# Optimization experiments

Hardware: AMD Instinct MI355X
Metric: run time of the kernel (lower is better)

Reference implementation:

```python
import jax, jax.numpy as jnp
import numpy as np

DIM = 768
HEADS = 12
SCALE = DIM ** (-0.5)  # NOTE: original scales by full dim, not per-head dim


def setup_inputs() -> dict:
    key = jax.random.key(0)
    k1, k2, k3 = jax.random.split(key, 3)
    b, n = 4, 2048
    x = jax.random.normal(k1, (b, n, DIM), dtype=jnp.float32)
    # torch Linear layout: weight [out_features, in_features]
    w_qkv = jax.random.normal(k2, (3 * DIM, DIM), dtype=jnp.float32) * (DIM ** -0.5)
    b_qkv = jnp.zeros((3 * DIM,), dtype=jnp.float32)
    w_out = jax.random.normal(k3, (DIM, DIM), dtype=jnp.float32) * (DIM ** -0.5)
    b_out = jnp.zeros((DIM,), dtype=jnp.float32)
    return {"x": x, "w_qkv": w_qkv, "b_qkv": b_qkv, "w_out": w_out, "b_out": b_out}


def reference(x, w_qkv, b_qkv, w_out, b_out):
    b, n, dim = x.shape
    h = HEADS
    d = dim // h
    qkv = x @ w_qkv.T + b_qkv                       # [b, n, 3*dim]
    # rearrange 'b n (qkv h d) -> qkv b h n d'
    qkv = qkv.reshape(b, n, 3, h, d).transpose(2, 0, 3, 1, 4)
    q, k, v = qkv[0], qkv[1], qkv[2]                # each [b, h, n, d]
    dots = jnp.einsum('bhid,bhjd->bhij', q, k) * SCALE
    attn = jax.nn.softmax(dots, axis=-1)
    out = jnp.einsum('bhij,bhjd->bhid', attn, v)    # [b, h, n, d]
    out = out.transpose(0, 2, 1, 3).reshape(b, n, h * d)
    out = out @ w_out.T + b_out
    return out
```

## Files before the change

kernel.cpp:

```cpp
#include <hip/hip_runtime.h>
#include <hip/hip_bf16.h>
#include <stdint.h>
#include <math.h>

#define HEADS 12
#define HD 64
#define NB 4
#define NSEQ 2048
#define DIM 768
#define MROWS (NB*NSEQ)
#define QKV_OUT (3*DIM)
#define QSCALE (0.03608439182435161f * 1.4426950408889634f)

typedef __bf16 bf16;
typedef __attribute__((ext_vector_type(8))) __bf16 bf16x8;
typedef __attribute__((ext_vector_type(4))) __bf16 bf16x4;
typedef __attribute__((ext_vector_type(4))) float f32x4;
typedef __attribute__((ext_vector_type(16))) float f32x16;
typedef unsigned int uint;

typedef __attribute__((address_space(1))) void gvoid_t;
typedef __attribute__((address_space(3))) void lvoid_t;
#define GLOAD_LDS16(src, dst) \
  __builtin_amdgcn_global_load_lds((gvoid_t*)(src), (lvoid_t*)(dst), 16, 0, 0)

__device__ __forceinline__ float fast_exp2(float x) {
  float r; asm("v_exp_f32 %0, %1" : "=v"(r) : "v"(x)); return r;
}
__device__ __forceinline__ uint cvtpk_bf16(float a, float b) {
  uint r; asm("v_cvt_pk_bf16_f32 %0, %1, %2" : "=v"(r) : "v"(a), "v"(b)); return r;
}
__device__ __forceinline__ void plswap(uint &a, uint &b) {
  asm("v_permlane32_swap_b32 %0, %1" : "+v"(a), "+v"(b));
}

__global__ void k_cvt3(const float* __restrict__ x, const float* __restrict__ wqkv,
                       const float* __restrict__ wout,
                       bf16* __restrict__ xb, bf16* __restrict__ wqkvb,
                       bf16* __restrict__ woutb) {
  const int n0 = MROWS * DIM / 4, n1 = QKV_OUT * DIM / 4, n2 = DIM * DIM / 4;
  int i = blockIdx.x * blockDim.x + threadIdx.x;
  const float* src; bf16* dst;
  if (i < n0)           { src = x;    dst = xb; }
  else if (i < n0 + n1) { src = wqkv; dst = wqkvb; i -= n0; }
  else if (i < n0 + n1 + n2) { src = wout; dst = woutb; i -= n0 + n1; }
  else return;
  const f32x4 v = ((const f32x4*)src)[i];
  bf16x4 o;
#pragma unroll
  for (int j = 0; j < 4; ++j) o[j] = (bf16)v[j];
  ((bf16x4*)dst)[i] = o;
}

template<int ROWBYTES>
__device__ __forceinline__ void stage_swz(const bf16* g, int grow0, int gstride,
                                          int gcol0, char* ldsbuf) {
  constexpr int CPR = ROWBYTES / 16;
  const int t = threadIdx.x;
  const int wid = t >> 6;
#pragma unroll
  for (int call = 0; call < 2; ++call) {
    const int o = call * 4096 + t * 16;
    const int r = o / ROWBYTES;
    const int c = (o % ROWBYTES) / 16;
    const int cs = c ^ (r & (CPR - 1));
    const bf16* src = g + (long)(grow0 + r) * gstride + gcol0 + cs * 8;
    char* dst = ldsbuf + call * 4096 + wid * 1024;
    GLOAD_LDS16(src, dst);
  }
}

template<int ROWBYTES>
__device__ __forceinline__ bf16x8 frag_ld(const char* buf, int row, int chunk) {
  constexpr int CPR = ROWBYTES / 16;
  const int cs = chunk ^ (row & (CPR - 1));
  return *(const bf16x8*)(buf + row * ROWBYTES + cs * 16);
}

__device__ __forceinline__ void build_pfrags(const f32x16 &p, bf16x8 *f) {
  union { uint u[4]; bf16x8 v; } A, B;
  uint a0 = cvtpk_bf16(p[0], p[1]),  b0 = cvtpk_bf16(p[4], p[5]);   plswap(a0, b0);
  uint a1 = cvtpk_bf16(p[2], p[3]),  b1 = cvtpk_bf16(p[6], p[7]);   plswap(a1, b1);
  A.u[0] = a0; A.u[1] = a1; A.u[2] = b0; A.u[3] = b1;
  uint a2 = cvtpk_bf16(p[8], p[9]),  b2 = cvtpk_bf16(p[12], p[13]); plswap(a2, b2);
  uint a3 = cvtpk_bf16(p[10], p[11]), b3 = cvtpk_bf16(p[14], p[15]); plswap(a3, b3);
  B.u[0] = a2; B.u[1] = a3; B.u[2] = b2; B.u[3] = b3;
  f[0] = A.v; f[1] = B.v;
}

__device__ __forceinline__ void gemm_core(const bf16* __restrict__ A, const bf16* __restrict__ Bm,
                                          int m0, int n0, f32x4 acc[4][4], char* lds) {
  const int t = threadIdx.x;
  const int lane = t & 63, wid = t >> 6;
  const int lr = lane & 15, l4 = lane >> 4;
  const int wm = wid >> 1, wn = wid & 1;
#pragma unroll
  for (int i = 0; i < 4; ++i)
#pragma unroll
    for (int j = 0; j < 4; ++j) acc[i][j] = f32x4{0.f, 0.f, 0.f, 0.f};

  stage_swz<64>(A, m0, DIM, 0, lds);
  stage_swz<64>(Bm, n0, DIM, 0, lds + 16384);
  __syncthreads();
  int cur = 0;
  const int NT = DIM / 32;
  for (int kt = 0; kt < NT; ++kt) {
    char* Acur = lds + cur * 8192;
    char* Bcur = lds + 16384 + cur * 8192;
    if (kt + 1 < NT) {
      stage_swz<64>(A, m0, DIM, (kt + 1) * 32, lds + (cur ^ 1) * 8192);
      stage_swz<64>(Bm, n0, DIM, (kt + 1) * 32, lds + 16384 + (cur ^ 1) * 8192);
    }
    bf16x8 af[4], bfr[4];
#pragma unroll
    for (int i = 0; i < 4; ++i) af[i] = frag_ld<64>(Acur, wm * 64 + i * 16 + lr, l4);
#pragma unroll
    for (int j = 0; j < 4; ++j) bfr[j] = frag_ld<64>(Bcur, wn * 64 + j * 16 + lr, l4);
#pragma unroll
    for (int i = 0; i < 4; ++i)
#pragma unroll
      for (int j = 0; j < 4; ++j)
        acc[i][j] = __builtin_amdgcn_mfma_f32_16x16x32_bf16(af[i], bfr[j], acc[i][j], 0, 0, 0);
    __syncthreads();
    cur ^= 1;
  }
}

__global__ void __launch_bounds__(256) k_qkv_gemm(const bf16* __restrict__ xb,
                                                  const bf16* __restrict__ wb,
                                                  const float* __restrict__ bqkv,
                                                  bf16* __restrict__ qb,
                                                  bf16* __restrict__ kb,
                                                  bf16* __restrict__ vtb) {
  __shared__ alignas(128) char lds[32768];
  const int m0 = blockIdx.x * 128;
  const int n0 = blockIdx.y * 128;
  const int region = n0 / DIM;
  const int t = threadIdx.x;
  const int lane = t & 63, wid = t >> 6;
  const int lr = lane & 15, l4 = lane >> 4;
  const int wm = wid >> 1, wn = wid & 1;
  f32x4 acc[4][4];

  if (region < 2) {
    gemm_core(wb, xb, n0, m0, acc, lds);
    bf16* dst0 = (region == 0) ? qb : kb;
#pragma unroll
    for (int j = 0; j < 4; ++j) {
      const int mb = m0 + wn * 64 + j * 16 + lr;
      const int bb = mb >> 11, nn = mb & 2047;
#pragma unroll
      for (int i = 0; i < 4; ++i) {
        const int o = n0 + wm * 64 + i * 16 + l4 * 4;
        const f32x4 b4 = *(const f32x4*)(bqkv + o);
        const int oc = o - region * DIM;
        const int h = oc >> 6, d = oc & 63;
        bf16x4 pk;
#pragma unroll
        for (int r = 0; r < 4; ++r) {
          float v = acc[i][j][r] + b4[r];
          if (region == 0) v *= QSCALE;
          pk[r] = (bf16)v;
        }
        *(bf16x4*)(dst0 + ((long)((bb * HEADS + h) * NSEQ + nn)) * HD + d) = pk;
      }
    }
  } else {
    gemm_core(xb, wb, m0, n0, acc, lds);
#pragma unroll
    for (int j = 0; j < 4; ++j) {
      const int o = n0 + wn * 64 + j * 16 + lr;
      const float bias = bqkv[o];
      const int oc = o - 2 * DIM;
      const int h = oc >> 6, d = oc & 63;
#pragma unroll
      for (int i = 0; i < 4; ++i) {
        const int mb = m0 + wm * 64 + i * 16 + l4 * 4;
        const int bb = mb >> 11, nn = mb & 2047;
        bf16x4 pk;
#pragma unroll
        for (int r = 0; r < 4; ++r) pk[r] = (bf16)(acc[i][j][r] + bias);
        *(bf16x4*)(vtb + ((long)((bb * HEADS + h) * HD + d)) * NSEQ + nn) = pk;
      }
    }
  }
}

__global__ void __launch_bounds__(256) k_attn(const bf16* __restrict__ qb,
                                              const bf16* __restrict__ kb,
                                              const bf16* __restrict__ vtb,
                                              bf16* __restrict__ ob) {
  __shared__ alignas(128) char lds[32768];
  char* ldsc = lds;
  const int bh = blockIdx.x;
  const int qt = blockIdx.y;
  const int t = threadIdx.x;
  const int lane = t & 63, wid = t >> 6;
  const int l31 = lane & 31, hi = lane >> 5;
  const bf16* qg = qb + (long)bh * NSEQ * HD;
  const bf16* kg = kb + (long)bh * NSEQ * HD;
  const bf16* vg = vtb + (long)bh * HD * NSEQ;
  const int q0w = qt * 128 + wid * 32;

  bf16x8 bq[4];
#pragma unroll
  for (int ks = 0; ks < 4; ++ks)
    bq[ks] = *(const bf16x8*)(qg + (long)(q0w + l31) * HD + ks * 16 + hi * 8);

  const int rbase = l31 * 128 + (((hi ^ l31) & 7) << 4);

  const int o0 = t * 16, o1 = 4096 + t * 16;
  const int r0 = o0 >> 7, cs0 = ((o0 & 127) >> 4) ^ (r0 & 7);
  const int r1 = o1 >> 7, cs1 = ((o1 & 127) >> 4) ^ (r1 & 7);
  const bf16* ksA = kg + r0 * 64 + cs0 * 8;
  const bf16* ksB = kg + r1 * 64 + cs1 * 8;
  const bf16* vsA = vg + (long)r0 * NSEQ + cs0 * 8;
  const bf16* vsB = vg + (long)r1 * NSEQ + cs1 * 8;
  const int dofs = wid << 10;

  f32x16 ot0, ot1;
#pragma unroll
  for (int r = 0; r < 16; ++r) { ot0[r] = 0.f; ot1[r] = 0.f; }
  float l_run = 0.f;

  GLOAD_LDS16(ksA, ldsc + dofs);
  GLOAD_LDS16(ksB, ldsc + 4096 + dofs);
  GLOAD_LDS16(vsA, ldsc + 16384 + dofs);
  GLOAD_LDS16(vsB, ldsc + 20480 + dofs);
  __syncthreads();
  int cur = 0;
  for (int kt = 0; kt < NSEQ / 64; ++kt) {
    if (kt + 1 < NSEQ / 64) {
      const int nb = (cur ^ 1) << 13;
      const int ko = (kt + 1) * 4096;
      const int vo = (kt + 1) * 64;
      GLOAD_LDS16(ksA + ko, ldsc + nb + dofs);
      GLOAD_LDS16(ksB + ko, ldsc + nb + 4096 + dofs);
      GLOAD_LDS16(vsA + vo, ldsc + nb + 16384 + dofs);
      GLOAD_LDS16(vsB + vo, ldsc + nb + 20480 + dofs);
    }
    const int tb = rbase + (cur << 13);
    f32x16 s0, s1;
#pragma unroll
    for (int r = 0; r < 16; ++r) { s0[r] = 0.f; s1[r] = 0.f; }
    __builtin_amdgcn_s_setprio(1);
#pragma unroll
    for (int ks = 0; ks < 4; ++ks) {
      const int a = tb ^ (ks << 5);
      const bf16x8 ak0 = *(const bf16x8*)(ldsc + a);
      s0 = __builtin_amdgcn_mfma_f32_32x32x16_bf16(ak0, bq[ks], s0, 0, 0, 0);
      const bf16x8 ak1 = *(const bf16x8*)(ldsc + a + 4096);
      s1 = __builtin_amdgcn_mfma_f32_32x32x16_bf16(ak1, bq[ks], s1, 0, 0, 0);
    }
    __builtin_amdgcn_s_setprio(0);
    float rs0 = 0.f, rs1 = 0.f;
#pragma unroll
    for (int r = 0; r < 16; ++r) {
      s0[r] = fast_exp2(s0[r]); rs0 += s0[r];
      s1[r] = fast_exp2(s1[r]); rs1 += s1[r];
    }
    l_run += rs0 + rs1;
    bf16x8 pf[4];
    build_pfrags(s0, &pf[0]);
    build_pfrags(s1, &pf[2]);
    __builtin_amdgcn_s_setprio(1);
#pragma unroll
    for (int s = 0; s < 4; ++s) {
      const int a = tb ^ (s << 5);
      const bf16x8 av0 = *(const bf16x8*)(ldsc + a + 16384);
      ot0 = __builtin_amdgcn_mfma_f32_32x32x16_bf16(av0, pf[s], ot0, 0, 0, 0);
      const bf16x8 av1 = *(const bf16x8*)(ldsc + a + 20480);
      ot1 = __builtin_amdgcn_mfma_f32_32x32x16_bf16(av1, pf[s], ot1, 0, 0, 0);
    }
    __builtin_amdgcn_s_setprio(0);
    __syncthreads();
    cur ^= 1;
  }
  l_run += __shfl_xor(l_run, 32);
  const float inv = 1.f / l_run;
#pragma unroll
  for (int r = 0; r < 16; ++r) { ot0[r] *= inv; ot1[r] *= inv; }
  __syncthreads();
  char* tw = lds + wid * 4352;
#pragma unroll
  for (int g = 0; g < 4; ++g) {
    uint2 w0, w1;
    w0.x = cvtpk_bf16(ot0[4 * g], ot0[4 * g + 1]);
    w0.y = cvtpk_bf16(ot0[4 * g + 2], ot0[4 * g + 3]);
    w1.x = cvtpk_bf16(ot1[4 * g], ot1[4 * g + 1]);
    w1.y = cvtpk_bf16(ot1[4 * g + 2], ot1[4 * g + 3]);
    const int d0 = 8 * g + 4 * hi;
    *(uint2*)(tw + l31 * 136 + d0 * 2) = w0;
    *(uint2*)(tw + l31 * 136 + (32 + d0) * 2) = w1;
  }
  const int b_ = bh / HEADS, h_ = bh - b_ * HEADS;
#pragma unroll
  for (int pass = 0; pass < 4; ++pass) {
    const int row = pass * 8 + (lane >> 3);
    const bf16x8 vv = *(const bf16x8*)(tw + row * 136 + (lane & 7) * 16);
    *(bf16x8*)(ob + ((long)(b_ * NSEQ + q0w + row)) * DIM + h_ * 64 + (lane & 7) * 8) = vv;
  }
}

__global__ void __launch_bounds__(256) k_out_gemm(const bf16* __restrict__ ab,
                                                  const bf16* __restrict__ wob,
                                                  const float* __restrict__ bout,
                                                  float* __restrict__ out) {
  __shared__ alignas(128) char lds[32768];
  const int m0 = blockIdx.x * 128;
  const int n0 = blockIdx.y * 128;
  f32x4 acc[4][4];
  gemm_core(wob, ab, n0, m0, acc, lds);

  const int t = threadIdx.x;
  const int lane = t & 63, wid = t >> 6;
  const int lr = lane & 15, l4 = lane >> 4;
  const int wm = wid >> 1, wn = wid & 1;
#pragma unroll
  for (int j = 0; j < 4; ++j) {
    const int mb = m0 + wn * 64 + j * 16 + lr;
#pragma unroll
    for (int i = 0; i < 4; ++i) {
      const int o = n0 + wm * 64 + i * 16 + l4 * 4;
      const f32x4 v = acc[i][j] + *(const f32x4*)(bout + o);
      *(f32x4*)(out + (long)mb * DIM + o) = v;
    }
  }
}

extern "C" void kernel_launch(void* const* d_in, const int* in_sizes, int n_in,
                              void* d_out, int out_size, void* d_ws, size_t ws_size,
                              hipStream_t stream) {
  const float* x    = (const float*)d_in[0];
  const float* wqkv = (const float*)d_in[1];
  const float* bqkv = (const float*)d_in[2];
  const float* wout = (const float*)d_in[3];
  const float* bout = (const float*)d_in[4];
  float* out = (float*)d_out;
  char* ws = (char*)d_ws;

  bf16* xb    = (bf16*)(ws);
  bf16* wqkvb = (bf16*)(ws + 12582912);
  bf16* woutb = (bf16*)(ws + 16121856);
  bf16* qb    = (bf16*)(ws + 17301504);
  bf16* kb    = (bf16*)(ws + 29884416);
  bf16* vtb   = (bf16*)(ws + 42467328);
  bf16* ab    = (bf16*)(ws + 55050240);

  const int ncvt4 = MROWS * DIM / 4 + QKV_OUT * DIM / 4 + DIM * DIM / 4;
  k_cvt3<<<(ncvt4 + 255) / 256, 256, 0, stream>>>(x, wqkv, wout, xb, wqkvb, woutb);

  k_qkv_gemm<<<dim3(MROWS / 128, QKV_OUT / 128), 256, 0, stream>>>(xb, wqkvb, bqkv, qb, kb, vtb);
  k_attn<<<dim3(NB * HEADS, NSEQ / 128), 256, 0, stream>>>(qb, kb, vtb, ab);
  k_out_gemm<<<dim3(MROWS / 128, DIM / 128), 256, 0, stream>>>(ab, woutb, bout, out);
}
```

Baseline: 153.0 us.

## Software-pipeline attention loop with triple-buffered K/V and overlapped QK^T

Restructures the attention kernel's main loop so the QK^T MFMAs for the next key tile are issued alongside the exp/PV work for the current tile. K and V now each get three LDS slots, with loads staged two or three tiles ahead under explicit vmcnt waits and raw barriers instead of full __syncthreads. The aim is to hide global-load latency and the softmax VALU work behind matrix work. In exchange, LDS per block grows from 32 KB to 48 KB and an extra pair of score accumulators raises register use, both of which can lower occupancy.

```diff
diff --git a/kernel.cpp b/kernel.cpp
--- a/kernel.cpp
+++ b/kernel.cpp
@@ -88,6 +88,47 @@
   f[0] = A.v; f[1] = B.v;
 }
 
+__device__ __forceinline__ void qkt_step(const char* ldsc, int rbase, int kslot,
+                                         const bf16x8 bq[4], f32x16 &P0, f32x16 &P1) {
+#pragma unroll
+  for (int r = 0; r < 16; ++r) { P0[r] = 0.f; P1[r] = 0.f; }
+  __builtin_amdgcn_s_setprio(1);
+#pragma unroll
+  for (int ks = 0; ks < 4; ++ks) {
+    const int a = (rbase ^ (ks << 5)) + kslot * 8192;
+    const bf16x8 ak0 = *(const bf16x8*)(ldsc + a);
+    P0 = __builtin_amdgcn_mfma_f32_32x32x16_bf16(ak0, bq[ks], P0, 0, 0, 0);
+    const bf16x8 ak1 = *(const bf16x8*)(ldsc + a + 4096);
+    P1 = __builtin_amdgcn_mfma_f32_32x32x16_bf16(ak1, bq[ks], P1, 0, 0, 0);
+  }
+  __builtin_amdgcn_s_setprio(0);
+}
+
+__device__ __forceinline__ void smpv_step(const char* ldsc, int rbase, int vslot,
+                                          f32x16 &C0, f32x16 &C1, f32x16 &ot0, f32x16 &ot1,
+                                          float &l_run) {
+  float rs0 = 0.f, rs1 = 0.f;
+#pragma unroll
+  for (int r = 0; r < 16; ++r) {
+    C0[r] = fast_exp2(C0[r]); rs0 += C0[r];
+    C1[r] = fast_exp2(C1[r]); rs1 += C1[r];
+  }
+  l_run += rs0 + rs1;
+  bf16x8 pf[4];
+  build_pfrags(C0, &pf[0]);
+  build_pfrags(C1, &pf[2]);
+  __builtin_amdgcn_s_setprio(1);
+#pragma unroll
+  for (int s = 0; s < 4; ++s) {
+    const int a = (rbase ^ (s << 5)) + 24576 + vslot * 8192;
+    const bf16x8 av0 = *(const bf16x8*)(ldsc + a);
+    ot0 = __builtin_amdgcn_mfma_f32_32x32x16_bf16(av0, pf[s], ot0, 0, 0, 0);
+    const bf16x8 av1 = *(const bf16x8*)(ldsc + a + 4096);
+    ot1 = __builtin_amdgcn_mfma_f32_32x32x16_bf16(av1, pf[s], ot1, 0, 0, 0);
+  }
+  __builtin_amdgcn_s_setprio(0);
+}
+
 __device__ __forceinline__ void gemm_core(const bf16* __restrict__ A, const bf16* __restrict__ Bm,
                                           int m0, int n0, f32x4 acc[4][4], char* lds) {
   const int t = threadIdx.x;
@@ -190,7 +231,7 @@
                                               const bf16* __restrict__ kb,
                                               const bf16* __restrict__ vtb,
                                               bf16* __restrict__ ob) {
-  __shared__ alignas(128) char lds[32768];
+  __shared__ alignas(128) char lds[49152];
   char* ldsc = lds;
   const int bh = blockIdx.x;
   const int qt = blockIdx.y;
@@ -210,77 +251,62 @@
   const int rbase = l31 * 128 + (((hi ^ l31) & 7) << 4);
 
   const int o0 = t * 16, o1 = 4096 + t * 16;
-  const int r0 = o0 >> 7, cs0 = ((o0 & 127) >> 4) ^ (r0 & 7);
-  const int r1 = o1 >> 7, cs1 = ((o1 & 127) >> 4) ^ (r1 & 7);
-  const bf16* ksA = kg + r0 * 64 + cs0 * 8;
-  const bf16* ksB = kg + r1 * 64 + cs1 * 8;
-  const bf16* vsA = vg + (long)r0 * NSEQ + cs0 * 8;
-  const bf16* vsB = vg + (long)r1 * NSEQ + cs1 * 8;
+  const int r0i = o0 >> 7, cs0 = ((o0 & 127) >> 4) ^ (r0i & 7);
+  const int r1i = o1 >> 7, cs1 = ((o1 & 127) >> 4) ^ (r1i & 7);
+  const bf16* ksA = kg + r0i * 64 + cs0 * 8;
+  const bf16* ksB = kg + r1i * 64 + cs1 * 8;
+  const bf16* vsA = vg + (long)r0i * NSEQ + cs0 * 8;
+  const bf16* vsB = vg + (long)r1i * NSEQ + cs1 * 8;
   const int dofs = wid << 10;
+
+  auto stage_k = [&](int j, int slot) {
+    GLOAD_LDS16(ksA + j * 4096, ldsc + slot * 8192 + dofs);
+    GLOAD_LDS16(ksB + j * 4096, ldsc + slot * 8192 + 4096 + dofs);
+  };
+  auto stage_v = [&](int j, int slot) {
+    GLOAD_LDS16(vsA + j * 64, ldsc + 24576 + slot * 8192 + dofs);
+    GLOAD_LDS16(vsB + j * 64, ldsc + 24576 + slot * 8192 + 4096 + dofs);
+  };
 
   f32x16 ot0, ot1;
 #pragma unroll
   for (int r = 0; r < 16; ++r) { ot0[r] = 0.f; ot1[r] = 0.f; }
   float l_run = 0.f;
 
-  GLOAD_LDS16(ksA, ldsc + dofs);
-  GLOAD_LDS16(ksB, ldsc + 4096 + dofs);
-  GLOAD_LDS16(vsA, ldsc + 16384 + dofs);
-  GLOAD_LDS16(vsB, ldsc + 20480 + dofs);
-  __syncthreads();
-  int cur = 0;
-  for (int kt = 0; kt < NSEQ / 64; ++kt) {
-    if (kt + 1 < NSEQ / 64) {
-      const int nb = (cur ^ 1) << 13;
-      const int ko = (kt + 1) * 4096;
-      const int vo = (kt + 1) * 64;
-      GLOAD_LDS16(ksA + ko, ldsc + nb + dofs);
-      GLOAD_LDS16(ksB + ko, ldsc + nb + 4096 + dofs);
-      GLOAD_LDS16(vsA + vo, ldsc + nb + 16384 + dofs);
-      GLOAD_LDS16(vsB + vo, ldsc + nb + 20480 + dofs);
-    }
-    const int tb = rbase + (cur << 13);
-    f32x16 s0, s1;
-#pragma unroll
-    for (int r = 0; r < 16; ++r) { s0[r] = 0.f; s1[r] = 0.f; }
-    __builtin_amdgcn_s_setprio(1);
-#pragma unroll
-    for (int ks = 0; ks < 4; ++ks) {
-      const int a = tb ^ (ks << 5);
-      const bf16x8 ak0 = *(const bf16x8*)(ldsc + a);
-      s0 = __builtin_amdgcn_mfma_f32_32x32x16_bf16(ak0, bq[ks], s0, 0, 0, 0);
-      const bf16x8 ak1 = *(const bf16x8*)(ldsc + a + 4096);
-      s1 = __builtin_amdgcn_mfma_f32_32x32x16_bf16(ak1, bq[ks], s1, 0, 0, 0);
-    }
-    __builtin_amdgcn_s_setprio(0);
-    float rs0 = 0.f, rs1 = 0.f;
-#pragma unroll
-    for (int r = 0; r < 16; ++r) {
-      s0[r] = fast_exp2(s0[r]); rs0 += s0[r];
-      s1[r] = fast_exp2(s1[r]); rs1 += s1[r];
-    }
-    l_run += rs0 + rs1;
-    bf16x8 pf[4];
-    build_pfrags(s0, &pf[0]);
-    build_pfrags(s1, &pf[2]);
-    __builtin_amdgcn_s_setprio(1);
-#pragma unroll
-    for (int s = 0; s < 4; ++s) {
-      const int a = tb ^ (s << 5);
-      const bf16x8 av0 = *(const bf16x8*)(ldsc + a + 16384);
-      ot0 = __builtin_amdgcn_mfma_f32_32x32x16_bf16(av0, pf[s], ot0, 0, 0, 0);
-      const bf16x8 av1 = *(const bf16x8*)(ldsc + a + 20480);
-      ot1 = __builtin_amdgcn_mfma_f32_32x32x16_bf16(av1, pf[s], ot1, 0, 0, 0);
-    }
-    __builtin_amdgcn_s_setprio(0);
-    __syncthreads();
-    cur ^= 1;
-  }
+  stage_k(0, 0);
+  asm volatile("s_waitcnt vmcnt(0)" ::: "memory");
+  __builtin_amdgcn_s_barrier();
+  asm volatile("" ::: "memory");
+  f32x16 sA0, sA1, sB0, sB1;
+  qkt_step(ldsc, rbase, 0, bq, sA0, sA1);
+  stage_k(1, 1); stage_v(0, 0);
+  stage_k(2, 2); stage_v(1, 1);
+
+  int s0r = 0, s1r = 1, s2r = 2;
+  auto iter = [&](int tt, f32x16 &C0, f32x16 &C1, f32x16 &P0, f32x16 &P1) {
+    asm volatile("s_waitcnt vmcnt(4)" ::: "memory");
+    __builtin_amdgcn_s_barrier();
+    asm volatile("" ::: "memory");
+    stage_k(tt + 3 < 32 ? tt + 3 : 31, s0r);
+    stage_v(tt + 2 < 32 ? tt + 2 : 31, s2r);
+    qkt_step(ldsc, rbase, s1r, bq, P0, P1);
+    smpv_step(ldsc, rbase, s0r, C0, C1, ot0, ot1, l_run);
+    int tmp = s0r; s0r = s1r; s1r = s2r; s2r = tmp;
+  };
+
+  for (int tp = 0; tp < 16; ++tp) {
+    iter(2 * tp, sA0, sA1, sB0, sB1);
+    if (tp < 15) iter(2 * tp + 1, sB0, sB1, sA0, sA1);
+  }
+  asm volatile("s_waitcnt vmcnt(0)" ::: "memory");
+  __builtin_amdgcn_s_barrier();
+  asm volatile("" ::: "memory");
+  smpv_step(ldsc, rbase, s0r, sB0, sB1, ot0, ot1, l_run);
+
   l_run += __shfl_xor(l_run, 32);
   const float inv = 1.f / l_run;
 #pragma unroll
   for (int r = 0; r < 16; ++r) { ot0[r] *= inv; ot1[r] *= inv; }
-  __syncthreads();
   char* tw = lds + wid * 4352;
 #pragma unroll
   for (int g = 0; g < 4; ++g) {
```

After: 147.8 us. 3.4% less time.
